# Optimization experiments

Hardware: AMD Instinct MI355X
Metric: run time of the kernel (lower is better)

The kernel has to match this reference:

```python
import jax, jax.numpy as jnp
import numpy as np

D_MODEL = 1024
NUM_HEADS = 16
HEAD_DIM = D_MODEL // NUM_HEADS
LN_EPS = 1e-3  # Keras LayerNormalization default epsilon


def setup_inputs() -> dict:
    key = jax.random.key(0)
    ks = jax.random.split(key, 7)
    s = 1.0 / np.sqrt(D_MODEL)
    return {
        "x": jax.random.normal(ks[0], (2, 2048, D_MODEL), dtype=jnp.float32),
        "Wq": jax.random.normal(ks[1], (D_MODEL, D_MODEL), dtype=jnp.float32) * s,
        "bq": jnp.zeros((D_MODEL,), dtype=jnp.float32),
        "Wk": jax.random.normal(ks[2], (D_MODEL, D_MODEL), dtype=jnp.float32) * s,
        "bk": jnp.zeros((D_MODEL,), dtype=jnp.float32),
        "Wv": jax.random.normal(ks[3], (D_MODEL, D_MODEL), dtype=jnp.float32) * s,
        "bv": jnp.zeros((D_MODEL,), dtype=jnp.float32),
        "ln_gamma": jnp.ones((D_MODEL,), dtype=jnp.float32),
        "ln_beta": jnp.zeros((D_MODEL,), dtype=jnp.float32),
    }


def _split_heads(t):
    # [B, S, D] -> [B, H, S, Dh]; matches tf.split(axis=2)+concat(axis=0) math
    B, S, D = t.shape
    return t.reshape(B, S, NUM_HEADS, HEAD_DIM).transpose(0, 2, 1, 3)


def reference(x, Wq, bq, Wk, bk, Wv, bv, ln_gamma, ln_beta):
    Q = _split_heads(x @ Wq + bq)   # [B,H,S,Dh]
    K = _split_heads(x @ Wk + bk)
    V = _split_heads(x @ Wv + bv)
    scale = 1.0 / jnp.sqrt(jnp.asarray(HEAD_DIM, dtype=x.dtype))
    scores = jnp.einsum("bhqd,bhkd->bhqk", Q, K) * scale
    probs = jax.nn.softmax(scores, axis=-1)  # dropout is identity at inference
    ctx = jnp.einsum("bhqk,bhkd->bhqd", probs, V)
    out = ctx.transpose(0, 2, 1, 3).reshape(x.shape)  # merge heads -> [B,S,D]
    out = out + x  # residual
    mean = jnp.mean(out, axis=-1, keepdims=True)
    var = jnp.mean(jnp.square(out - mean), axis=-1, keepdims=True)
    return (out - mean) * jax.lax.rsqrt(var + LN_EPS) * ln_gamma + ln_beta
```

## Files before the change

kernel.cpp:

```cpp
#include <hip/hip_runtime.h>
#include <stdint.h>

#define D_MODEL 1024
#define SEQ     2048
#define BATCH   2
#define NHEADS  16
#define HDIM    64
#define ROWS    (BATCH*SEQ)

typedef __attribute__((ext_vector_type(8)))  short short8;
typedef __attribute__((ext_vector_type(4)))  float f32x4;
typedef __attribute__((ext_vector_type(16))) float f32x16;
typedef __attribute__((ext_vector_type(4)))  short short4v;

__device__ __forceinline__ unsigned short f2bf(float f){
  union { float f; unsigned int u; } v; v.f = f;
  unsigned int r = v.u + 0x7fffu + ((v.u >> 16) & 1u);
  return (unsigned short)(r >> 16);
}

__device__ __forceinline__ float fast_exp2(float x){
  float r;
  asm("v_exp_f32 %0, %1" : "=v"(r) : "v"(x));
  return r;
}

__device__ __forceinline__ float f3(float a, float b, float c){
  return fmaxf(fmaxf(a,b),c);
}

__device__ __forceinline__ void gload16(const void* g, void* l){
  __builtin_amdgcn_global_load_lds((__attribute__((address_space(1))) void*)(uintptr_t)g,
                                   (__attribute__((address_space(3))) void*)l, 16, 0, 0);
}

__global__ __launch_bounds__(256) void prep(const float* __restrict__ x,
                                            const float* __restrict__ Wq,
                                            const float* __restrict__ Wk,
                                            const float* __restrict__ Wv,
                                            unsigned short* __restrict__ xb,
                                            unsigned short* __restrict__ Wt){
  __shared__ float tile[32][33];
  const int bidx = blockIdx.x;
  if (bidx < 4096){
    const int i = bidx*256 + threadIdx.x;
    float4 v = ((const float4*)x)[i];
    short4v o;
    o[0] = (short)f2bf(v.x); o[1] = (short)f2bf(v.y);
    o[2] = (short)f2bf(v.z); o[3] = (short)f2bf(v.w);
    ((short4v*)xb)[i] = o;
  } else {
    const int wz  = bidx - 4096;
    const int mat = wz >> 10;
    const int idx = wz & 1023;
    const float* W = (mat==0)?Wq:((mat==1)?Wk:Wv);
    unsigned short* dst = Wt + (size_t)mat*1048576;
    const int tx = threadIdx.x & 31, ty = threadIdx.x >> 5;
    const int n0 = (idx & 31)*32, k0 = (idx >> 5)*32;
    #pragma unroll
    for (int j=0;j<32;j+=8)
      tile[ty+j][tx] = W[(size_t)(k0+ty+j)*D_MODEL + n0+tx];
    __syncthreads();
    #pragma unroll
    for (int j=0;j<32;j+=8)
      dst[(size_t)(n0+ty+j)*D_MODEL + k0+tx] = f2bf(tile[tx][ty+j]);
  }
}

__global__ __launch_bounds__(256) void qkv_gemm(
    const unsigned short* __restrict__ xb, const unsigned short* __restrict__ wtb,
    const float* __restrict__ bq, const float* __restrict__ bk, const float* __restrict__ bv,
    unsigned short* __restrict__ qb, unsigned short* __restrict__ kbuf,
    unsigned short* __restrict__ vbuf)
{
  __shared__ unsigned short As[2][128*32];
  __shared__ unsigned short Bs[2][128*32];
  const int mat = blockIdx.z;
  const unsigned short* wt = wtb + (size_t)mat*1048576;
  const float* bias = (mat==0)?bq:((mat==1)?bk:bv);
  unsigned short* outp = (mat==0)?qb:((mat==1)?kbuf:vbuf);
  const float osc = (mat==0)?0.18033688011112042f:1.0f;
  const int bm = blockIdx.x, bn = blockIdx.y;
  const int t = threadIdx.x, w = t>>6, lane = t&63;
  const int g = lane>>4, l15 = lane&15;
  const int wm = w>>1, wn = w&1;

  const int srow = (w<<5) + (lane>>2);
  const int scol = (lane&3)*8;

  f32x4 acc[4][4];
  #pragma unroll
  for (int i=0;i<4;++i)
    #pragma unroll
    for (int j=0;j<4;++j) acc[i][j] = (f32x4){0.f,0.f,0.f,0.f};

#define QSTAGE(buf, kt) do {                                                       \
    const int k0 = (kt)*32;                                                        \
    gload16(xb + (size_t)(bm*128 + srow)*D_MODEL      + k0 + scol, &As[buf][(w<<10)]);        \
    gload16(xb + (size_t)(bm*128 + srow + 16)*D_MODEL + k0 + scol, &As[buf][(w<<10)+(1<<9)]); \
    gload16(wt + (size_t)(bn*128 + srow)*D_MODEL      + k0 + scol, &Bs[buf][(w<<10)]);        \
    gload16(wt + (size_t)(bn*128 + srow + 16)*D_MODEL + k0 + scol, &Bs[buf][(w<<10)+(1<<9)]); \
  } while(0)

  QSTAGE(0, 0);
  __syncthreads();
  int cur = 0;
  for (int kt=0; kt<32; ++kt){
    if (kt < 31) QSTAGE(cur^1, kt+1);
    short8 a[4], b[4];
    #pragma unroll
    for (int mr=0;mr<4;++mr) a[mr] = *(const short8*)&As[cur][(wm*64 + mr*16 + l15)*32 + g*8];
    #pragma unroll
    for (int nr=0;nr<4;++nr) b[nr] = *(const short8*)&Bs[cur][(wn*64 + nr*16 + l15)*32 + g*8];
    __builtin_amdgcn_s_setprio(1);
    #pragma unroll
    for (int mr=0;mr<4;++mr)
      #pragma unroll
      for (int nr=0;nr<4;++nr)
        acc[mr][nr] = __builtin_amdgcn_mfma_f32_16x16x32_bf16(a[mr], b[nr], acc[mr][nr], 0,0,0);
    __builtin_amdgcn_s_setprio(0);
    if (kt < 31){ __syncthreads(); cur ^= 1; }
  }
#undef QSTAGE

  #pragma unroll
  for (int mr=0;mr<4;++mr){
    const int rowb = bm*128 + wm*64 + mr*16 + g*4;
    #pragma unroll
    for (int nr=0;nr<4;++nr){
      const int col = bn*128 + wn*64 + nr*16 + l15;
      const float bsv = bias[col];
      const int h = col>>6, d = col&63;
      #pragma unroll
      for (int r=0;r<4;++r){
        const int m = rowb + r;
        const int b_ = m>>11, s = m&2047;
        outp[(((size_t)(b_*NHEADS + h))*SEQ + s)*HDIM + d] = f2bf((acc[mr][nr][r] + bsv)*osc);
      }
    }
  }
}

__global__ __launch_bounds__(256) void vtrans(const unsigned short* __restrict__ vb,
                                              unsigned short* __restrict__ vt){
  __shared__ unsigned short tile[64*72];
  const int bh = blockIdx.y;
  const int s0 = blockIdx.x*64;
  const int t = threadIdx.x;
  {
    const int s_loc = t>>2, d0 = (t&3)*16;
    const unsigned short* src = vb + ((size_t)bh*SEQ + s0 + s_loc)*HDIM + d0;
    *(short8*)&tile[s_loc*72 + d0]     = *(const short8*)src;
    *(short8*)&tile[s_loc*72 + d0 + 8] = *(const short8*)(src+8);
  }
  __syncthreads();
  {
    const int d = t>>2, sc = (t&3)*16;
    short8 o0, o1;
    #pragma unroll
    for (int j=0;j<8;++j){
      o0[j] = (short)tile[(sc+j)*72 + d];
      o1[j] = (short)tile[(sc+8+j)*72 + d];
    }
    unsigned short* dst = vt + ((size_t)bh*HDIM + d)*SEQ + s0 + sc;
    *(short8*)dst     = o0;
    *(short8*)(dst+8) = o1;
  }
}

__global__ __launch_bounds__(256, 2) void attn_fwd(
  const unsigned short* __restrict__ Qb, const unsigned short* __restrict__ Kb,
  const unsigned short* __restrict__ Vtb, float* __restrict__ ctx)
{
  __shared__ unsigned short Ks[2][4096];
  __shared__ unsigned short Vs[2][4096];
  const int lin = blockIdx.x;
  const int bh = (lin&7)*4 + (lin>>7);
  const int q0 = ((lin>>3)&15)*128;
  const int t = threadIdx.x, w = t>>6, lane = t&63;
  const int l31 = lane&31, hi = lane>>5;
  const unsigned short* Qh  = Qb  + (size_t)bh*SEQ*HDIM;
  const unsigned short* Kh  = Kb  + (size_t)bh*SEQ*HDIM;
  const unsigned short* Vth = Vtb + (size_t)bh*HDIM*SEQ;

  const int qrow = q0 + w*32 + l31;
  short8 qf[4];
  #pragma unroll
  for (int dht=0;dht<4;++dht)
    qf[dht] = *(const short8*)&Qh[(size_t)qrow*HDIM + dht*16 + hi*8];

  const int srow0 = t>>3,        srow1 = (256+t)>>3;
  const int skk0  = ((t&7)<<3) ^ ((srow0&7)<<3);
  const int skk1  = ((t&7)<<3) ^ ((srow1&7)<<3);
  const int rx    = l31&7;

  float m = 0.f;
  float rsum = 0.f;
  f32x16 o0, o1;
  #pragma unroll
  for (int r=0;r<16;++r){ o0[r]=0.f; o1[r]=0.f; }

#define STAGE(buf, ktile) do {                                                    \
    const int kb_ = (ktile)*64;                                                   \
    gload16(&Kh[(size_t)(kb_ + srow0)*HDIM + skk0], &Ks[buf][(w*64)*8]);          \
    gload16(&Kh[(size_t)(kb_ + srow1)*HDIM + skk1], &Ks[buf][(256 + w*64)*8]);    \
    gload16(&Vth[(size_t)srow0*SEQ + kb_ + skk0],   &Vs[buf][(w*64)*8]);          \
    gload16(&Vth[(size_t)srow1*SEQ + kb_ + skk1],   &Vs[buf][(256 + w*64)*8]);    \
  } while(0)

#define BODY(CUR, KT, FIRST) do {                                                 \
    if ((KT) < 31) STAGE((CUR)^1, (KT)+1);                                        \
                                       \
    f32x16 s0, s1;                                                                \
    _Pragma("unroll")                                                             \
    for (int r=0;r<16;++r){ s0[r]=0.f; s1[r]=0.f; }                               \
    __builtin_amdgcn_s_setprio(1);                                                \
    _Pragma("unroll")                                                             \
    for (int dht=0;dht<4;++dht){                                                  \
      short8 kf = *(const short8*)&Ks[CUR][l31*64 + (((dht<<1)|hi) ^ rx)*8];      \
      s0 = __builtin_amdgcn_mfma_f32_32x32x16_bf16(kf, qf[dht], s0, 0,0,0);       \
    }                                                                             \
    _Pragma("unroll")                                                             \
    for (int dht=0;dht<4;++dht){                                                  \
      short8 kf = *(const short8*)&Ks[CUR][(32+l31)*64 + (((dht<<1)|hi) ^ rx)*8]; \
      s1 = __builtin_amdgcn_mfma_f32_32x32x16_bf16(kf, qf[dht], s1, 0,0,0);       \
    }                                                                             \
    __builtin_amdgcn_s_setprio(0);                                                \
    if (FIRST){                                                                   \
      float a0=f3(s0[0],s0[1],s0[2]),  a1=f3(s0[3],s0[4],s0[5]);                  \
      float a2=f3(s0[6],s0[7],s0[8]),  a3=f3(s0[9],s0[10],s0[11]);                \
      float a4=f3(s0[12],s0[13],s0[14]), a5=f3(s0[15],s1[0],s1[1]);               \
      float a6=f3(s1[2],s1[3],s1[4]),  a7=f3(s1[5],s1[6],s1[7]);                  \
      float a8=f3(s1[8],s1[9],s1[10]), a9=f3(s1[11],s1[12],s1[13]);               \
      float a10=fmaxf(s1[14],s1[15]);                                             \
      float rmx = f3(f3(a0,a1,a2), f3(a3,a4,a5), f3(f3(a6,a7,a8), a9, a10));      \
      m = fmaxf(rmx, __shfl_xor(rmx, 32));                                        \
    }                                                                             \
          \
    unsigned int u[8], vv[8];                                                     \
    _Pragma("unroll")                                                             \
    for (int i=0;i<8;++i){                                                        \
      float e0 = fast_exp2(s0[2*i]   - m);                                        \
      float e1 = fast_exp2(s0[2*i+1] - m);                                        \
      float e2 = fast_exp2(s1[2*i]   - m);                                        \
      float e3 = fast_exp2(s1[2*i+1] - m);                                        \
      rsum += (e0+e1)+(e2+e3);                                                    \
      asm("v_cvt_pk_bf16_f32 %0, %1, %2" : "=v"(u[i])  : "v"(e0), "v"(e1));       \
      asm("v_cvt_pk_bf16_f32 %0, %1, %2" : "=v"(vv[i]) : "v"(e2), "v"(e3));       \
    }                                                                             \
    asm("v_permlane32_swap_b32 %0, %1" : "+v"(u[0]),  "+v"(u[2]));                \
    asm("v_permlane32_swap_b32 %0, %1" : "+v"(u[1]),  "+v"(u[3]));                \
    asm("v_permlane32_swap_b32 %0, %1" : "+v"(u[4]),  "+v"(u[6]));                \
    asm("v_permlane32_swap_b32 %0, %1" : "+v"(u[5]),  "+v"(u[7]));                \
    asm("v_permlane32_swap_b32 %0, %1" : "+v"(vv[0]), "+v"(vv[2]));               \
    asm("v_permlane32_swap_b32 %0, %1" : "+v"(vv[1]), "+v"(vv[3]));               \
    asm("v_permlane32_swap_b32 %0, %1" : "+v"(vv[4]), "+v"(vv[6]));               \
    asm("v_permlane32_swap_b32 %0, %1" : "+v"(vv[5]), "+v"(vv[7]));               \
    union U8 { unsigned int wq[4]; short8 s; };                                   \
    short8 pa[4];                                                                 \
    { U8 x; x.wq[0]=u[0];  x.wq[1]=u[1];  x.wq[2]=u[2];  x.wq[3]=u[3];  pa[0]=x.s; } \
    { U8 x; x.wq[0]=u[4];  x.wq[1]=u[5];  x.wq[2]=u[6];  x.wq[3]=u[7];  pa[1]=x.s; } \
    { U8 x; x.wq[0]=vv[0]; x.wq[1]=vv[1]; x.wq[2]=vv[2]; x.wq[3]=vv[3]; pa[2]=x.s; } \
    { U8 x; x.wq[0]=vv[4]; x.wq[1]=vv[5]; x.wq[2]=vv[6]; x.wq[3]=vv[7]; pa[3]=x.s; } \
                                                                    \
    __builtin_amdgcn_s_setprio(1);                                                \
    _Pragma("unroll")                                                             \
    for (int kb=0;kb<4;++kb){                                                     \
      short8 vf0 = *(const short8*)&Vs[CUR][l31*64      + (((kb<<1)|hi) ^ rx)*8]; \
      short8 vf1 = *(const short8*)&Vs[CUR][(32+l31)*64 + (((kb<<1)|hi) ^ rx)*8]; \
      o0 = __builtin_amdgcn_mfma_f32_32x32x16_bf16(pa[kb], vf0, o0, 0,0,0);       \
      o1 = __builtin_amdgcn_mfma_f32_32x32x16_bf16(pa[kb], vf1, o1, 0,0,0);       \
    }                                                                             \
    __builtin_amdgcn_s_setprio(0);                                                \
    if ((KT) < 31) __syncthreads();                                               \
  } while(0)

  STAGE(0, 0);
  __syncthreads();

  BODY(0, 0, 1);
  BODY(1, 1, 0);
  for (int kt2=2; kt2<32; kt2+=2){
    BODY(0, kt2,   0);
    BODY(1, kt2+1, 0);
  }
#undef BODY
#undef STAGE

  const float rst = rsum + __shfl_xor(rsum, 32);
  const int b_ = bh>>4, h = bh&15;
  #pragma unroll
  for (int r=0;r<16;++r){
    const int cr = (r&3) + ((r>>2)<<3) + (hi<<2);
    const float inv = 1.0f / __shfl(rst, cr);
    const int s = q0 + w*32 + cr;
    float* dst = &ctx[((size_t)(b_*SEQ + s))*D_MODEL + h*64];
    dst[l31]      = o0[r] * inv;
    dst[32 + l31] = o1[r] * inv;
  }
}

__global__ __launch_bounds__(256) void resid_ln(
  const float* __restrict__ ctx, const float* __restrict__ x,
  const float* __restrict__ gamma, const float* __restrict__ beta,
  float* __restrict__ out)
{
  const int row = blockIdx.x, t = threadIdx.x;
  const size_t base = (size_t)row*D_MODEL;
  float4 c  = ((const float4*)(ctx + base))[t];
  float4 xr = ((const float4*)(x   + base))[t];
  float4 v; v.x=c.x+xr.x; v.y=c.y+xr.y; v.z=c.z+xr.z; v.w=c.w+xr.w;
  float s  = v.x+v.y+v.z+v.w;
  float ss = v.x*v.x+v.y*v.y+v.z*v.z+v.w*v.w;
  #pragma unroll
  for (int m=1;m<64;m<<=1){ s += __shfl_xor(s,m); ss += __shfl_xor(ss,m); }
  __shared__ float red[8];
  const int w = t>>6;
  if ((t&63)==0){ red[w] = s; red[4+w] = ss; }
  __syncthreads();
  s  = red[0]+red[1]+red[2]+red[3];
  ss = red[4]+red[5]+red[6]+red[7];
  const float mean = s*(1.f/D_MODEL);
  const float var  = ss*(1.f/D_MODEL) - mean*mean;
  const float rstd = rsqrtf(var + 1e-3f);
  float4 gv = ((const float4*)gamma)[t], bv = ((const float4*)beta)[t];
  float4 ov;
  ov.x=(v.x-mean)*rstd*gv.x+bv.x; ov.y=(v.y-mean)*rstd*gv.y+bv.y;
  ov.z=(v.z-mean)*rstd*gv.z+bv.z; ov.w=(v.w-mean)*rstd*gv.w+bv.w;
  ((float4*)(out + base))[t] = ov;
}

extern "C" void kernel_launch(void* const* d_in, const int* in_sizes, int n_in,
                              void* d_out, int out_size, void* d_ws, size_t ws_size,
                              hipStream_t stream){
  const float* x     = (const float*)d_in[0];
  const float* Wq    = (const float*)d_in[1];
  const float* bq    = (const float*)d_in[2];
  const float* Wk    = (const float*)d_in[3];
  const float* bk    = (const float*)d_in[4];
  const float* Wv    = (const float*)d_in[5];
  const float* bv    = (const float*)d_in[6];
  const float* gamma = (const float*)d_in[7];
  const float* beta  = (const float*)d_in[8];
  float* out = (float*)d_out;

  char* ws = (char*)d_ws;
  unsigned short* xb  = (unsigned short*)(ws);
  unsigned short* wtb = (unsigned short*)(ws + 8388608);
  unsigned short* qb  = (unsigned short*)(ws + 14680064);
  unsigned short* kb  = (unsigned short*)(ws + 23068672);
  unsigned short* vb  = (unsigned short*)(ws + 31457280);
  float* ctx          = (float*)(ws + 39845888);
  unsigned short* vtb = (unsigned short*)(ws);

  hipLaunchKernelGGL(prep,     dim3(7168),              dim3(256), 0, stream,
                     x, Wq, Wk, Wv, xb, wtb);
  hipLaunchKernelGGL(qkv_gemm, dim3(32,8,3),            dim3(256), 0, stream,
                     xb, wtb, bq, bk, bv, qb, kb, vb);
  hipLaunchKernelGGL(vtrans,   dim3(SEQ/64, BATCH*NHEADS), dim3(256), 0, stream, vb, vtb);
  hipLaunchKernelGGL(attn_fwd, dim3(512),               dim3(256), 0, stream, qb, kb, vtb, ctx);
  hipLaunchKernelGGL(resid_ln, dim3(ROWS),              dim3(256), 0, stream, ctx, x, gamma, beta, out);
}
```

Measured before the change: 111.1 us.

## Double attention K/V tile to 128 keys and unroll projection GEMM loop

The attention kernel now stages 128 keys per tile instead of 64 and processes each tile as two 64-key halves. This halves the number of barriers and prefetch rounds, at the cost of doubling the K/V LDS footprint (64KB per block), which may limit occupancy. The V-transpose layout and swizzle are rewritten to match the 128-wide rows. The QKV projection loop is manually unrolled by two with constant buffer indices, and its setprio hints are removed.

```diff
diff --git a/kernel.cpp b/kernel.cpp
--- a/kernel.cpp
+++ b/kernel.cpp
@@ -102,25 +102,29 @@
     gload16(wt + (size_t)(bn*128 + srow + 16)*D_MODEL + k0 + scol, &Bs[buf][(w<<10)+(1<<9)]); \
   } while(0)
 
+#define QBODY(CUR, KT) do {                                                        \
+    if ((KT) < 31) QSTAGE((CUR)^1, (KT)+1);                                        \
+    short8 a[4], b[4];                                                             \
+    _Pragma("unroll")                                                              \
+    for (int mr=0;mr<4;++mr) a[mr] = *(const short8*)&As[CUR][(wm*64 + mr*16 + l15)*32 + g*8]; \
+    _Pragma("unroll")                                                              \
+    for (int nr=0;nr<4;++nr) b[nr] = *(const short8*)&Bs[CUR][(wn*64 + nr*16 + l15)*32 + g*8]; \
+    _Pragma("unroll")                                                              \
+    for (int mr=0;mr<4;++mr)                                                       \
+      _Pragma("unroll")                                                            \
+      for (int nr=0;nr<4;++nr)                                                     \
+        acc[mr][nr] = __builtin_amdgcn_mfma_f32_16x16x32_bf16(a[mr], b[nr], acc[mr][nr], 0,0,0); \
+    if ((KT) < 31) __syncthreads();                                                \
+  } while(0)
+
   QSTAGE(0, 0);
   __syncthreads();
-  int cur = 0;
-  for (int kt=0; kt<32; ++kt){
-    if (kt < 31) QSTAGE(cur^1, kt+1);
-    short8 a[4], b[4];
-    #pragma unroll
-    for (int mr=0;mr<4;++mr) a[mr] = *(const short8*)&As[cur][(wm*64 + mr*16 + l15)*32 + g*8];
-    #pragma unroll
-    for (int nr=0;nr<4;++nr) b[nr] = *(const short8*)&Bs[cur][(wn*64 + nr*16 + l15)*32 + g*8];
-    __builtin_amdgcn_s_setprio(1);
-    #pragma unroll
-    for (int mr=0;mr<4;++mr)
-      #pragma unroll
-      for (int nr=0;nr<4;++nr)
-        acc[mr][nr] = __builtin_amdgcn_mfma_f32_16x16x32_bf16(a[mr], b[nr], acc[mr][nr], 0,0,0);
-    __builtin_amdgcn_s_setprio(0);
-    if (kt < 31){ __syncthreads(); cur ^= 1; }
-  }
+  #pragma unroll 1
+  for (int ktt=0; ktt<16; ++ktt){
+    QBODY(0, 2*ktt);
+    QBODY(1, 2*ktt+1);
+  }
+#undef QBODY
 #undef QSTAGE
 
   #pragma unroll
@@ -172,8 +176,8 @@
   const unsigned short* __restrict__ Qb, const unsigned short* __restrict__ Kb,
   const unsigned short* __restrict__ Vtb, float* __restrict__ ctx)
 {
-  __shared__ unsigned short Ks[2][4096];
-  __shared__ unsigned short Vs[2][4096];
+  __shared__ unsigned short Ks[2][128*64];
+  __shared__ unsigned short Vs[2][64*128];
   const int lin = blockIdx.x;
   const int bh = (lin&7)*4 + (lin>>7);
   const int q0 = ((lin>>3)&15)*128;
@@ -189,10 +193,14 @@
   for (int dht=0;dht<4;++dht)
     qf[dht] = *(const short8*)&Qh[(size_t)qrow*HDIM + dht*16 + hi*8];
 
-  const int srow0 = t>>3,        srow1 = (256+t)>>3;
-  const int skk0  = ((t&7)<<3) ^ ((srow0&7)<<3);
-  const int skk1  = ((t&7)<<3) ^ ((srow1&7)<<3);
-  const int rx    = l31&7;
+  int krow[4], kchk[4], vrow[4], vchk[4];
+  #pragma unroll
+  for (int j=0;j<4;++j){
+    const int i = j*256 + t;
+    krow[j] = i>>3;  kchk[j] = (((i&7) ^ (krow[j]&7))<<3);
+    vrow[j] = i>>4;  vchk[j] = ((((i&15) ^ (vrow[j]&7)))<<3);
+  }
+  const int rx = l31&7;
 
   float m = 0.f;
   float rsum = 0.f;
@@ -201,28 +209,28 @@
   for (int r=0;r<16;++r){ o0[r]=0.f; o1[r]=0.f; }
 
 #define STAGE(buf, ktile) do {                                                    \
-    const int kb_ = (ktile)*64;                                                   \
-    gload16(&Kh[(size_t)(kb_ + srow0)*HDIM + skk0], &Ks[buf][(w*64)*8]);          \
-    gload16(&Kh[(size_t)(kb_ + srow1)*HDIM + skk1], &Ks[buf][(256 + w*64)*8]);    \
-    gload16(&Vth[(size_t)srow0*SEQ + kb_ + skk0],   &Vs[buf][(w*64)*8]);          \
-    gload16(&Vth[(size_t)srow1*SEQ + kb_ + skk1],   &Vs[buf][(256 + w*64)*8]);    \
-  } while(0)
-
-#define BODY(CUR, KT, FIRST) do {                                                 \
-    if ((KT) < 31) STAGE((CUR)^1, (KT)+1);                                        \
-                                       \
+    const int kb_ = (ktile)*128;                                                  \
+    _Pragma("unroll")                                                             \
+    for (int j=0;j<4;++j)                                                         \
+      gload16(&Kh[(size_t)(kb_ + krow[j])*HDIM + kchk[j]], &Ks[buf][(j*256 + t - lane)*8]); \
+    _Pragma("unroll")                                                             \
+    for (int j=0;j<4;++j)                                                         \
+      gload16(&Vth[(size_t)vrow[j]*SEQ + kb_ + vchk[j]],   &Vs[buf][(j*256 + t - lane)*8]); \
+  } while(0)
+
+#define HALF(CUR, H, FIRST) do {                                                  \
     f32x16 s0, s1;                                                                \
     _Pragma("unroll")                                                             \
     for (int r=0;r<16;++r){ s0[r]=0.f; s1[r]=0.f; }                               \
     __builtin_amdgcn_s_setprio(1);                                                \
     _Pragma("unroll")                                                             \
     for (int dht=0;dht<4;++dht){                                                  \
-      short8 kf = *(const short8*)&Ks[CUR][l31*64 + (((dht<<1)|hi) ^ rx)*8];      \
+      short8 kf = *(const short8*)&Ks[CUR][((H)*64 + l31)*64 + (((dht<<1)|hi) ^ rx)*8]; \
       s0 = __builtin_amdgcn_mfma_f32_32x32x16_bf16(kf, qf[dht], s0, 0,0,0);       \
     }                                                                             \
     _Pragma("unroll")                                                             \
     for (int dht=0;dht<4;++dht){                                                  \
-      short8 kf = *(const short8*)&Ks[CUR][(32+l31)*64 + (((dht<<1)|hi) ^ rx)*8]; \
+      short8 kf = *(const short8*)&Ks[CUR][((H)*64 + 32 + l31)*64 + (((dht<<1)|hi) ^ rx)*8]; \
       s1 = __builtin_amdgcn_mfma_f32_32x32x16_bf16(kf, qf[dht], s1, 0,0,0);       \
     }                                                                             \
     __builtin_amdgcn_s_setprio(0);                                                \
@@ -236,7 +244,6 @@
       float rmx = f3(f3(a0,a1,a2), f3(a3,a4,a5), f3(f3(a6,a7,a8), a9, a10));      \
       m = fmaxf(rmx, __shfl_xor(rmx, 32));                                        \
     }                                                                             \
-          \
     unsigned int u[8], vv[8];                                                     \
     _Pragma("unroll")                                                             \
     for (int i=0;i<8;++i){                                                        \
@@ -262,17 +269,23 @@
     { U8 x; x.wq[0]=u[4];  x.wq[1]=u[5];  x.wq[2]=u[6];  x.wq[3]=u[7];  pa[1]=x.s; } \
     { U8 x; x.wq[0]=vv[0]; x.wq[1]=vv[1]; x.wq[2]=vv[2]; x.wq[3]=vv[3]; pa[2]=x.s; } \
     { U8 x; x.wq[0]=vv[4]; x.wq[1]=vv[5]; x.wq[2]=vv[6]; x.wq[3]=vv[7]; pa[3]=x.s; } \
-                                                                    \
     __builtin_amdgcn_s_setprio(1);                                                \
     _Pragma("unroll")                                                             \
     for (int kb=0;kb<4;++kb){                                                     \
-      short8 vf0 = *(const short8*)&Vs[CUR][l31*64      + (((kb<<1)|hi) ^ rx)*8]; \
-      short8 vf1 = *(const short8*)&Vs[CUR][(32+l31)*64 + (((kb<<1)|hi) ^ rx)*8]; \
+      const int vc = (((H)<<3) | (((kb<<1)|hi) ^ rx))*8;                          \
+      short8 vf0 = *(const short8*)&Vs[CUR][l31*128      + vc];                   \
+      short8 vf1 = *(const short8*)&Vs[CUR][(32+l31)*128 + vc];                   \
       o0 = __builtin_amdgcn_mfma_f32_32x32x16_bf16(pa[kb], vf0, o0, 0,0,0);       \
       o1 = __builtin_amdgcn_mfma_f32_32x32x16_bf16(pa[kb], vf1, o1, 0,0,0);       \
     }                                                                             \
     __builtin_amdgcn_s_setprio(0);                                                \
-    if ((KT) < 31) __syncthreads();                                               \
+  } while(0)
+
+#define BODY(CUR, KT, FIRST) do {                                                 \
+    if ((KT) < 15) STAGE((CUR)^1, (KT)+1);                                        \
+    HALF(CUR, 0, FIRST);                                                          \
+    HALF(CUR, 1, 0);                                                              \
+    if ((KT) < 15) __syncthreads();                                               \
   } while(0)
 
   STAGE(0, 0);
@@ -280,11 +293,13 @@
 
   BODY(0, 0, 1);
   BODY(1, 1, 0);
-  for (int kt2=2; kt2<32; kt2+=2){
+  #pragma unroll 1
+  for (int kt2=2; kt2<16; kt2+=2){
     BODY(0, kt2,   0);
     BODY(1, kt2+1, 0);
   }
 #undef BODY
+#undef HALF
 #undef STAGE
 
   const float rst = rsum + __shfl_xor(rsum, 32);
```

Result: slower. 122.8 us (+10.6%).

## Fuse V transpose into QKV GEMM epilogue and drop LDS double buffering

Applied to the files above, without the earlier changes.

The QKV GEMM epilogue now writes V directly in transposed [b,h,d,s] layout, which removes the separate vtrans kernel launch and its extra read/write pass over V. The GEMM main loop also drops its double-buffered LDS prefetch and the s_setprio hints. It now loads each K-tile synchronously, with two barriers per iteration. The transposed V stores are strided by SEQ, so they coalesce poorly, and losing the prefetch exposes global load latency in the GEMM.

```diff
diff --git a/kernel.cpp b/kernel.cpp
--- a/kernel.cpp
+++ b/kernel.cpp
@@ -71,14 +71,13 @@
     const unsigned short* __restrict__ xb, const unsigned short* __restrict__ wtb,
     const float* __restrict__ bq, const float* __restrict__ bk, const float* __restrict__ bv,
     unsigned short* __restrict__ qb, unsigned short* __restrict__ kbuf,
-    unsigned short* __restrict__ vbuf)
+    unsigned short* __restrict__ vtb)
 {
-  __shared__ unsigned short As[2][128*32];
-  __shared__ unsigned short Bs[2][128*32];
+  __shared__ unsigned short As[128*32];
+  __shared__ unsigned short Bs[128*32];
   const int mat = blockIdx.z;
   const unsigned short* wt = wtb + (size_t)mat*1048576;
   const float* bias = (mat==0)?bq:((mat==1)?bk:bv);
-  unsigned short* outp = (mat==0)?qb:((mat==1)?kbuf:vbuf);
   const float osc = (mat==0)?0.18033688011112042f:1.0f;
   const int bm = blockIdx.x, bn = blockIdx.y;
   const int t = threadIdx.x, w = t>>6, lane = t&63;
@@ -94,35 +93,26 @@
     #pragma unroll
     for (int j=0;j<4;++j) acc[i][j] = (f32x4){0.f,0.f,0.f,0.f};
 
-#define QSTAGE(buf, kt) do {                                                       \
-    const int k0 = (kt)*32;                                                        \
-    gload16(xb + (size_t)(bm*128 + srow)*D_MODEL      + k0 + scol, &As[buf][(w<<10)]);        \
-    gload16(xb + (size_t)(bm*128 + srow + 16)*D_MODEL + k0 + scol, &As[buf][(w<<10)+(1<<9)]); \
-    gload16(wt + (size_t)(bn*128 + srow)*D_MODEL      + k0 + scol, &Bs[buf][(w<<10)]);        \
-    gload16(wt + (size_t)(bn*128 + srow + 16)*D_MODEL + k0 + scol, &Bs[buf][(w<<10)+(1<<9)]); \
-  } while(0)
-
-  QSTAGE(0, 0);
-  __syncthreads();
-  int cur = 0;
   for (int kt=0; kt<32; ++kt){
-    if (kt < 31) QSTAGE(cur^1, kt+1);
+    const int k0 = kt*32;
+    #pragma unroll
+    for (int j=0;j<2;++j){
+      gload16(xb + (size_t)(bm*128 + srow + j*16)*D_MODEL + k0 + scol, &As[(w<<10)+(j<<9)]);
+      gload16(wt + (size_t)(bn*128 + srow + j*16)*D_MODEL + k0 + scol, &Bs[(w<<10)+(j<<9)]);
+    }
+    __syncthreads();
     short8 a[4], b[4];
     #pragma unroll
-    for (int mr=0;mr<4;++mr) a[mr] = *(const short8*)&As[cur][(wm*64 + mr*16 + l15)*32 + g*8];
-    #pragma unroll
-    for (int nr=0;nr<4;++nr) b[nr] = *(const short8*)&Bs[cur][(wn*64 + nr*16 + l15)*32 + g*8];
-    __builtin_amdgcn_s_setprio(1);
+    for (int mr=0;mr<4;++mr) a[mr] = *(const short8*)&As[(wm*64 + mr*16 + l15)*32 + g*8];
+    #pragma unroll
+    for (int nr=0;nr<4;++nr) b[nr] = *(const short8*)&Bs[(wn*64 + nr*16 + l15)*32 + g*8];
     #pragma unroll
     for (int mr=0;mr<4;++mr)
       #pragma unroll
       for (int nr=0;nr<4;++nr)
         acc[mr][nr] = __builtin_amdgcn_mfma_f32_16x16x32_bf16(a[mr], b[nr], acc[mr][nr], 0,0,0);
-    __builtin_amdgcn_s_setprio(0);
-    if (kt < 31){ __syncthreads(); cur ^= 1; }
-  }
-#undef QSTAGE
-
+    __syncthreads();
+  }
   #pragma unroll
   for (int mr=0;mr<4;++mr){
     const int rowb = bm*128 + wm*64 + mr*16 + g*4;
@@ -135,36 +125,15 @@
       for (int r=0;r<4;++r){
         const int m = rowb + r;
         const int b_ = m>>11, s = m&2047;
-        outp[(((size_t)(b_*NHEADS + h))*SEQ + s)*HDIM + d] = f2bf((acc[mr][nr][r] + bsv)*osc);
+        const unsigned short val = f2bf((acc[mr][nr][r] + bsv)*osc);
+        if (mat==2)
+          vtb [(((size_t)(b_*NHEADS + h))*HDIM + d)*SEQ + s] = val;
+        else if (mat==0)
+          qb  [(((size_t)(b_*NHEADS + h))*SEQ + s)*HDIM + d] = val;
+        else
+          kbuf[(((size_t)(b_*NHEADS + h))*SEQ + s)*HDIM + d] = val;
       }
     }
-  }
-}
-
-__global__ __launch_bounds__(256) void vtrans(const unsigned short* __restrict__ vb,
-                                              unsigned short* __restrict__ vt){
-  __shared__ unsigned short tile[64*72];
-  const int bh = blockIdx.y;
-  const int s0 = blockIdx.x*64;
-  const int t = threadIdx.x;
-  {
-    const int s_loc = t>>2, d0 = (t&3)*16;
-    const unsigned short* src = vb + ((size_t)bh*SEQ + s0 + s_loc)*HDIM + d0;
-    *(short8*)&tile[s_loc*72 + d0]     = *(const short8*)src;
-    *(short8*)&tile[s_loc*72 + d0 + 8] = *(const short8*)(src+8);
-  }
-  __syncthreads();
-  {
-    const int d = t>>2, sc = (t&3)*16;
-    short8 o0, o1;
-    #pragma unroll
-    for (int j=0;j<8;++j){
-      o0[j] = (short)tile[(sc+j)*72 + d];
-      o1[j] = (short)tile[(sc+8+j)*72 + d];
-    }
-    unsigned short* dst = vt + ((size_t)bh*HDIM + d)*SEQ + s0 + sc;
-    *(short8*)dst     = o0;
-    *(short8*)(dst+8) = o1;
   }
 }
 
@@ -349,15 +318,13 @@
   unsigned short* wtb = (unsigned short*)(ws + 8388608);
   unsigned short* qb  = (unsigned short*)(ws + 14680064);
   unsigned short* kb  = (unsigned short*)(ws + 23068672);
-  unsigned short* vb  = (unsigned short*)(ws + 31457280);
+  unsigned short* vtb = (unsigned short*)(ws + 31457280);
   float* ctx          = (float*)(ws + 39845888);
-  unsigned short* vtb = (unsigned short*)(ws);
 
   hipLaunchKernelGGL(prep,     dim3(7168),              dim3(256), 0, stream,
                      x, Wq, Wk, Wv, xb, wtb);
   hipLaunchKernelGGL(qkv_gemm, dim3(32,8,3),            dim3(256), 0, stream,
-                     xb, wtb, bq, bk, bv, qb, kb, vb);
-  hipLaunchKernelGGL(vtrans,   dim3(SEQ/64, BATCH*NHEADS), dim3(256), 0, stream, vb, vtb);
+                     xb, wtb, bq, bk, bv, qb, kb, vtb);
   hipLaunchKernelGGL(attn_fwd, dim3(512),               dim3(256), 0, stream, qb, kb, vtb, ctx);
   hipLaunchKernelGGL(resid_ln, dim3(ROWS),              dim3(256), 0, stream, ctx, x, gamma, beta, out);
 }
```

Result: no change. 109.5 us (-1.5%).
